# Optimization experiments

Hardware: AMD Instinct MI355X
Metric: run time of the kernel (lower is better)

Reference implementation:

```python
import jax, jax.numpy as jnp
import numpy as np

B, S, H, NH = 2, 2048, 1024, 16
HD = H // NH


def setup_inputs() -> dict:
    key = jax.random.key(0)
    ks = jax.random.split(key, 12)
    inp = {
        "query": jax.random.normal(ks[0], (B, S, H), dtype=jnp.float32),
        "key": jax.random.normal(ks[1], (B, S, H), dtype=jnp.float32),
        "value": jax.random.normal(ks[2], (B, S, H), dtype=jnp.float32),
        "mask": jnp.ones((B, 1, S, S), dtype=jnp.int32),
        "script_mask": jax.random.uniform(ks[3], (B, S, S), dtype=jnp.float32),
    }
    scale = 1.0 / np.sqrt(H)
    inp["Wq"] = jax.random.normal(ks[4], (H, H), dtype=jnp.float32) * scale
    inp["bq"] = jnp.zeros((H,), dtype=jnp.float32)
    inp["Wk"] = jax.random.normal(ks[5], (H, H), dtype=jnp.float32) * scale
    inp["bk"] = jnp.zeros((H,), dtype=jnp.float32)
    inp["Wv"] = jax.random.normal(ks[6], (H, H), dtype=jnp.float32) * scale
    inp["bv"] = jnp.zeros((H,), dtype=jnp.float32)
    inp["Wo"] = jax.random.normal(ks[7], (H, H), dtype=jnp.float32) * scale
    inp["bo"] = jnp.zeros((H,), dtype=jnp.float32)
    return inp


def reference(query, key, value, mask, script_mask, Wq, bq, Wk, bk, Wv, bv, Wo, bo):
    b, s, h = query.shape
    # projections; torch Linear: x @ W.T + b
    q = (query @ Wq.T + bq).reshape(b, s, NH, HD).transpose(0, 2, 1, 3)  # [b,nh,s,hd]
    k = (key @ Wk.T + bk).reshape(b, s, NH, HD).transpose(0, 2, 1, 3)
    v = (value @ Wv.T + bv).reshape(b, s, NH, HD).transpose(0, 2, 1, 3)
    scores = jnp.einsum("bhqd,bhkd->bhqk", q, k) / jnp.sqrt(jnp.float32(HD))
    # multiplicative script mask, broadcast over heads
    scores = scores * script_mask[:, None, :, :]
    # additive mask: positions where mask == 0 -> -inf
    scores = jnp.where(mask == 0, -jnp.inf, scores)
    attn = jax.nn.softmax(scores, axis=-1)
    out = jnp.einsum("bhqk,bhkd->bhqd", attn, v)  # [b,nh,s,hd]
    out = out.transpose(0, 2, 1, 3).reshape(b, s, h)
    return out @ Wo.T + bo
```

## Files before the change

kernel.cpp:

```cpp
#include <hip/hip_runtime.h>
#include <stdint.h>

#define NH 16
#define SEQ 2048
#define HDIM 1024

typedef short bf16x8 __attribute__((ext_vector_type(8)));
typedef float f32x4 __attribute__((ext_vector_type(4)));
typedef float f32x2 __attribute__((ext_vector_type(2)));

#define NEG_BIG (-1.0e30f)

static __device__ __forceinline__ uint32_t cvtpk_bf16(float lo, float hi) {
  uint32_t r;
  asm("v_cvt_pk_bf16_f32 %0, %1, %2" : "=v"(r) : "v"(lo), "v"(hi));
  return r;
}
static __device__ __forceinline__ uint16_t f2bf(float f) {
  return (uint16_t)cvtpk_bf16(f, f);
}
static __device__ __forceinline__ f32x2 pk_mul(f32x2 a, f32x2 b) {
  f32x2 d;
  asm("v_pk_mul_f32 %0, %1, %2" : "=v"(d) : "v"(a), "v"(b));
  return d;
}
static __device__ __forceinline__ f32x2 pk_add(f32x2 a, f32x2 b) {
  f32x2 d;
  asm("v_pk_add_f32 %0, %1, %2" : "=v"(d) : "v"(a), "v"(b));
  return d;
}
static __device__ __forceinline__ float bitf(uint32_t u) {
  return __builtin_bit_cast(float, u);
}

struct CvtArgs {
  const float* src[7];
  uint16_t* dst[7];
  int nblk[7];
};
__global__ __launch_bounds__(256) void cvt_bf16(CvtArgs a) {
  int ten = blockIdx.y;
  if (blockIdx.x >= a.nblk[ten]) return;
  size_t idx = ((size_t)blockIdx.x * 256 + threadIdx.x) * 8;
  const float* s = a.src[ten] + idx;
  float4 f0 = *(const float4*)(s);
  float4 f1 = *(const float4*)(s + 4);
  uint4 o;
  o.x = cvtpk_bf16(f0.x, f0.y);
  o.y = cvtpk_bf16(f0.z, f0.w);
  o.z = cvtpk_bf16(f1.x, f1.y);
  o.w = cvtpk_bf16(f1.z, f1.w);
  *(uint4*)(a.dst[ten] + idx) = o;
}

__global__ __launch_bounds__(256) void cm_prep(const int4* __restrict__ mask,
                                               const float4* __restrict__ sm,
                                               uint4* __restrict__ cm) {
  int i = blockIdx.x * 256 + threadIdx.x;
  int4 m0 = mask[2 * i];
  int4 m1 = mask[2 * i + 1];
  float4 s0 = sm[2 * i];
  float4 s1 = sm[2 * i + 1];
  const float cst = 0.18033688011112042f;
  auto pk = [&](int mA, int mB, float fa, float fb) -> uint32_t {
    float a = mA ? fa * cst : -1.0f;
    float b = mB ? fb * cst : -1.0f;
    return cvtpk_bf16(a, b);
  };
  uint4 o;
  o.x = pk(m0.x, m0.y, s0.x, s0.y);
  o.y = pk(m0.z, m0.w, s0.z, s0.w);
  o.z = pk(m1.x, m1.y, s1.x, s1.y);
  o.w = pk(m1.z, m1.w, s1.z, s1.w);
  cm[i] = o;
}

struct GemmArgs {
  const uint16_t* A[4];
  const uint16_t* B[4];
  const float* bias[4];
  void* C[4];
};

#define LDA 40

__global__ __launch_bounds__(256) void gemm_bt(GemmArgs ga, int modeBase) {
  int mode = modeBase + blockIdx.y;
  const uint16_t* __restrict__ A = ga.A[mode];
  const uint16_t* __restrict__ Bm = ga.B[mode];
  const float* __restrict__ bias = ga.bias[mode];

  int bid = blockIdx.x;
  int tm, tn;
  if (mode == 2) { tm = bid & 7; tn = bid >> 3; }
  else           { tm = bid >> 3; tn = bid & 7; }

  __shared__ uint16_t As[128 * LDA];
  __shared__ uint16_t Bs[128 * LDA];

  int t = threadIdx.x;
  int lane = t & 63, w = t >> 6;
  int quad = lane >> 4, lm = lane & 15;
  int wm = w >> 1, wn = w & 1;

  const uint16_t* Ab = A + (size_t)tm * 128 * 1024;
  const uint16_t* Bb = Bm + (size_t)tn * 128 * 1024;
  int srow = w * 32 + (lane >> 2);
  int scol = (lane & 3) * 8;

  f32x4 acc[4][4] = {};

  for (int kk = 0; kk < 1024; kk += 32) {
    uint4 a0 = *(const uint4*)(Ab + (size_t)srow * 1024 + kk + scol);
    uint4 a1 = *(const uint4*)(Ab + (size_t)(srow + 16) * 1024 + kk + scol);
    uint4 b0 = *(const uint4*)(Bb + (size_t)srow * 1024 + kk + scol);
    uint4 b1 = *(const uint4*)(Bb + (size_t)(srow + 16) * 1024 + kk + scol);
    __syncthreads();
    *(uint4*)&As[srow * LDA + scol] = a0;
    *(uint4*)&As[(srow + 16) * LDA + scol] = a1;
    *(uint4*)&Bs[srow * LDA + scol] = b0;
    *(uint4*)&Bs[(srow + 16) * LDA + scol] = b1;
    __syncthreads();

    bf16x8 af[4], bfr[4];
#pragma unroll
    for (int i = 0; i < 4; i++)
      af[i] = *(const bf16x8*)&As[(wm * 64 + i * 16 + lm) * LDA + quad * 8];
#pragma unroll
    for (int j = 0; j < 4; j++)
      bfr[j] = *(const bf16x8*)&Bs[(wn * 64 + j * 16 + lm) * LDA + quad * 8];
#pragma unroll
    for (int i = 0; i < 4; i++)
#pragma unroll
      for (int j = 0; j < 4; j++)
        acc[i][j] = __builtin_amdgcn_mfma_f32_16x16x32_bf16(af[i], bfr[j], acc[i][j], 0, 0, 0);
  }

  int rowb = tm * 128 + wm * 64;
  int colb = tn * 128 + wn * 64;
#pragma unroll
  for (int i = 0; i < 4; i++) {
#pragma unroll
    for (int j = 0; j < 4; j++) {
      int col = colb + j * 16 + lm;
#pragma unroll
      for (int r = 0; r < 4; r++) {
        int row = rowb + i * 16 + quad * 4 + r;
        float v = acc[i][j][r];
        if (mode == 2) {
          v += bias[row];
          int hh = row >> 6, hd = row & 63, b = col >> 11, s2 = col & 2047;
          ((uint16_t*)ga.C[2])[((size_t)((b * NH + hh) * 64 + hd) << 11) + s2] = f2bf(v);
        } else if (mode == 3) {
          v += bias[col];
          ((float*)ga.C[3])[(size_t)row * 1024 + col] = v;
        } else {
          v += bias[col];
          int b = row >> 11, s2 = row & 2047, hh = col >> 6, hd = col & 63;
          ((uint16_t*)ga.C[mode])[(((size_t)(b * NH + hh) * 2048 + s2) << 6) + hd] = f2bf(v);
        }
      }
    }
  }
}

#define LDK 72

__global__ __launch_bounds__(256) void attn(const uint16_t* __restrict__ qp,
                                            const uint16_t* __restrict__ kp,
                                            const uint16_t* __restrict__ vt,
                                            const uint16_t* __restrict__ cm,
                                            uint16_t* __restrict__ ao) {
  int h = blockIdx.x, qt = blockIdx.y, b = blockIdx.z;
  int t = threadIdx.x;
  int lane = t & 63, w = t >> 6;
  int quad = lane >> 4, c = lane & 15;

  __shared__ uint16_t Ks[64 * LDK];
  __shared__ uint16_t VTs[64 * LDK];
  __shared__ uint16_t Ps[64 * LDK];

  size_t bh = (size_t)(b * NH + h);
  const uint16_t* Kb = kp + bh * (SEQ * 64);
  const uint16_t* Vb = vt + bh * (64 * SEQ);
  const uint16_t* CMb = cm + ((size_t)b * SEQ + qt * 64) * SEQ;

  int qrow = qt * 64 + w * 16 + c;
  const uint16_t* Qb = qp + bh * (SEQ * 64) + (size_t)qrow * 64;
  bf16x8 qf0 = *(const bf16x8*)(Qb + quad * 8);
  bf16x8 qf1 = *(const bf16x8*)(Qb + 32 + quad * 8);

  f32x4 Oacc[4] = {};
  float m_run = NEG_BIG;
  float l_run = 0.0f;

  int krow = w * 8 + (lane >> 3);
  int kc = (lane & 7) * 8;

  const uint16_t* pK0 = Kb + (size_t)krow * 64 + kc;
  const uint16_t* pK1 = pK0 + 32 * 64;
  const uint16_t* pV0 = Vb + (size_t)krow * SEQ + kc;
  const uint16_t* pV1 = pV0 + (size_t)32 * SEQ;
  const uint16_t* pCM = CMb + (size_t)(w * 16 + c) * SEQ + quad * 4;

  uint16_t* sK0 = &Ks[krow * LDK + kc];
  uint16_t* sK1 = sK0 + 32 * LDK;
  uint16_t* sV0 = &VTs[krow * LDK + kc];
  uint16_t* sV1 = sV0 + 32 * LDK;

  const uint16_t* rK = &Ks[c * LDK];
  const uint16_t* rV = &VTs[c * LDK];
  uint16_t* sP = &Ps[(w * 16 + c) * LDK];
  int qo = quad * 8;

  auto compute = [&](uint2 c0, uint2 c1, uint2 c2, uint2 c3) {
    f32x4 st[4];
    __builtin_amdgcn_s_setprio(1);
#pragma unroll
    for (int i = 0; i < 4; i++) {
      bf16x8 a0 = *(const bf16x8*)(rK + i * 16 * LDK + qo);
      bf16x8 a1 = *(const bf16x8*)(rK + i * 16 * LDK + 32 + qo);
      f32x4 z = {};
      z = __builtin_amdgcn_mfma_f32_16x16x32_bf16(a0, qf0, z, 0, 0, 0);
      st[i] = __builtin_amdgcn_mfma_f32_16x16x32_bf16(a1, qf1, z, 0, 0, 0);
    }
    __builtin_amdgcn_s_setprio(0);

    const f32x2 big2 = {1.0e30f, 1.0e30f};
    f32x2 pp[8];
    float tmax = NEG_BIG;
    const uint2 cmv[4] = {c0, c1, c2, c3};
#pragma unroll
    for (int i = 0; i < 4; i++) {
      uint32_t w0 = cmv[i].x, w1 = cmv[i].y;
      f32x2 cf01 = {bitf(w0 << 16), bitf(w0 & 0xffff0000u)};
      f32x2 cf23 = {bitf(w1 << 16), bitf(w1 & 0xffff0000u)};
      f32x2 s01 = {st[i][0], st[i][1]};
      f32x2 s23 = {st[i][2], st[i][3]};
      f32x2 m01 = pk_mul(s01, cf01), q01 = pk_mul(big2, cf01);
      f32x2 m23 = pk_mul(s23, cf23), q23 = pk_mul(big2, cf23);
      f32x2 r01 = {fminf(m01.x, q01.x), fminf(m01.y, q01.y)};
      f32x2 r23 = {fminf(m23.x, q23.x), fminf(m23.y, q23.y)};
      pp[2 * i] = r01;
      pp[2 * i + 1] = r23;
      tmax = fmaxf(tmax, fmaxf(fmaxf(r01.x, r01.y), fmaxf(r23.x, r23.y)));
    }
    tmax = fmaxf(tmax, __shfl_xor(tmax, 16));
    tmax = fmaxf(tmax, __shfl_xor(tmax, 32));
    if (!__all(tmax <= m_run + 8.0f)) {
      float m_new = fmaxf(m_run, tmax);
      float alpha = exp2f(m_run - m_new);
      m_run = m_new;
      l_run *= alpha;
#pragma unroll
      for (int i = 0; i < 4; i++) Oacc[i] *= alpha;
    }
    f32x2 mneg = {-m_run, -m_run};
    f32x2 acc2 = {0.0f, 0.0f};
#pragma unroll
    for (int j = 0; j < 8; j++) {
      f32x2 e = pk_add(pp[j], mneg);
      pp[j].x = exp2f(e.x);
      pp[j].y = exp2f(e.y);
      acc2 = pk_add(acc2, pp[j]);
    }
    l_run += acc2.x + acc2.y;

#pragma unroll
    for (int i = 0; i < 4; i++) {
      uint2 pkd;
      pkd.x = cvtpk_bf16(pp[2 * i].x, pp[2 * i].y);
      pkd.y = cvtpk_bf16(pp[2 * i + 1].x, pp[2 * i + 1].y);
      *(uint2*)(sP + i * 16 + quad * 4) = pkd;
    }
    asm volatile("s_waitcnt lgkmcnt(0)" ::: "memory");
    __builtin_amdgcn_sched_barrier(0);

    bf16x8 pf0 = *(const bf16x8*)(sP + qo);
    bf16x8 pf1 = *(const bf16x8*)(sP + 32 + qo);
    __builtin_amdgcn_s_setprio(1);
#pragma unroll
    for (int i = 0; i < 4; i++) {
      bf16x8 v0 = *(const bf16x8*)(rV + i * 16 * LDK + qo);
      bf16x8 v1 = *(const bf16x8*)(rV + i * 16 * LDK + 32 + qo);
      Oacc[i] = __builtin_amdgcn_mfma_f32_16x16x32_bf16(v0, pf0, Oacc[i], 0, 0, 0);
      Oacc[i] = __builtin_amdgcn_mfma_f32_16x16x32_bf16(v1, pf1, Oacc[i], 0, 0, 0);
    }
    __builtin_amdgcn_s_setprio(0);
  };

  uint4 rk0 = *(const uint4*)(pK0), rk1 = *(const uint4*)(pK1);
  uint4 rv0 = *(const uint4*)(pV0), rv1 = *(const uint4*)(pV1);
  uint2 cA0 = *(const uint2*)(pCM);
  uint2 cA1 = *(const uint2*)(pCM + 16);
  uint2 cA2 = *(const uint2*)(pCM + 32);
  uint2 cA3 = *(const uint2*)(pCM + 48);
  pK0 += 64 * 64; pK1 += 64 * 64; pV0 += 64; pV1 += 64; pCM += 64;
  uint2 cB0, cB1, cB2, cB3;

  for (int it = 0; it < SEQ / 128; ++it) {
    __syncthreads();
    *(uint4*)sK0 = rk0;
    *(uint4*)sK1 = rk1;
    *(uint4*)sV0 = rv0;
    *(uint4*)sV1 = rv1;
    __syncthreads();
    rk0 = *(const uint4*)(pK0); rk1 = *(const uint4*)(pK1);
    rv0 = *(const uint4*)(pV0); rv1 = *(const uint4*)(pV1);
    cB0 = *(const uint2*)(pCM);
    cB1 = *(const uint2*)(pCM + 16);
    cB2 = *(const uint2*)(pCM + 32);
    cB3 = *(const uint2*)(pCM + 48);
    pK0 += 64 * 64; pK1 += 64 * 64; pV0 += 64; pV1 += 64; pCM += 64;
    compute(cA0, cA1, cA2, cA3);
    __syncthreads();
    *(uint4*)sK0 = rk0;
    *(uint4*)sK1 = rk1;
    *(uint4*)sV0 = rv0;
    *(uint4*)sV1 = rv1;
    __syncthreads();
    if (it < SEQ / 128 - 1) {
      rk0 = *(const uint4*)(pK0); rk1 = *(const uint4*)(pK1);
      rv0 = *(const uint4*)(pV0); rv1 = *(const uint4*)(pV1);
      cA0 = *(const uint2*)(pCM);
      cA1 = *(const uint2*)(pCM + 16);
      cA2 = *(const uint2*)(pCM + 32);
      cA3 = *(const uint2*)(pCM + 48);
      pK0 += 64 * 64; pK1 += 64 * 64; pV0 += 64; pV1 += 64; pCM += 64;
    }
    compute(cB0, cB1, cB2, cB3);
  }

  float lf = l_run + __shfl_xor(l_run, 16);
  lf = lf + __shfl_xor(lf, 32);
  float inv = 1.0f / lf;
  uint16_t* Ob = ao + ((size_t)(b * SEQ) + qt * 64 + w * 16 + c) * HDIM + h * 64;
#pragma unroll
  for (int i = 0; i < 4; i++) {
    uint2 ov;
    ov.x = cvtpk_bf16(Oacc[i][0] * inv, Oacc[i][1] * inv);
    ov.y = cvtpk_bf16(Oacc[i][2] * inv, Oacc[i][3] * inv);
    *(uint2*)(Ob + i * 16 + quad * 4) = ov;
  }
}

extern "C" void kernel_launch(void* const* d_in, const int* in_sizes, int n_in,
                              void* d_out, int out_size, void* d_ws, size_t ws_size,
                              hipStream_t stream) {
  (void)in_sizes; (void)n_in; (void)out_size; (void)ws_size;
  const float* query = (const float*)d_in[0];
  const float* key   = (const float*)d_in[1];
  const float* value = (const float*)d_in[2];
  const int*   mask  = (const int*)d_in[3];
  const float* smask = (const float*)d_in[4];
  const float* Wq = (const float*)d_in[5];
  const float* bq = (const float*)d_in[6];
  const float* Wk = (const float*)d_in[7];
  const float* bk = (const float*)d_in[8];
  const float* Wv = (const float*)d_in[9];
  const float* bv = (const float*)d_in[10];
  const float* Wo = (const float*)d_in[11];
  const float* bo = (const float*)d_in[12];

  char* p = (char*)d_ws;
  uint16_t* xq  = (uint16_t*)p; p += (size_t)2 * SEQ * HDIM * 2;
  uint16_t* xk  = (uint16_t*)p; p += (size_t)2 * SEQ * HDIM * 2;
  uint16_t* xv  = (uint16_t*)p; p += (size_t)2 * SEQ * HDIM * 2;
  uint16_t* wqb = (uint16_t*)p; p += (size_t)HDIM * HDIM * 2;
  uint16_t* wkb = (uint16_t*)p; p += (size_t)HDIM * HDIM * 2;
  uint16_t* wvb = (uint16_t*)p; p += (size_t)HDIM * HDIM * 2;
  uint16_t* wob = (uint16_t*)p; p += (size_t)HDIM * HDIM * 2;
  uint16_t* qp  = (uint16_t*)p; p += (size_t)2 * NH * SEQ * 64 * 2;
  uint16_t* kpp = (uint16_t*)p; p += (size_t)2 * NH * SEQ * 64 * 2;
  uint16_t* vtp = (uint16_t*)p; p += (size_t)2 * NH * SEQ * 64 * 2;
  uint16_t* cmw = (uint16_t*)p; p += (size_t)2 * SEQ * SEQ * 2;
  uint16_t* aob = (uint16_t*)p; p += (size_t)2 * SEQ * HDIM * 2;

  CvtArgs ca;
  ca.src[0] = query; ca.dst[0] = xq;  ca.nblk[0] = 2048;
  ca.src[1] = key;   ca.dst[1] = xk;  ca.nblk[1] = 2048;
  ca.src[2] = value; ca.dst[2] = xv;  ca.nblk[2] = 2048;
  ca.src[3] = Wq;    ca.dst[3] = wqb; ca.nblk[3] = 512;
  ca.src[4] = Wk;    ca.dst[4] = wkb; ca.nblk[4] = 512;
  ca.src[5] = Wv;    ca.dst[5] = wvb; ca.nblk[5] = 512;
  ca.src[6] = Wo;    ca.dst[6] = wob; ca.nblk[6] = 512;
  cvt_bf16<<<dim3(2048, 7), 256, 0, stream>>>(ca);

  cm_prep<<<4096, 256, 0, stream>>>((const int4*)mask, (const float4*)smask, (uint4*)cmw);

  GemmArgs ga;
  ga.A[0] = xq;  ga.B[0] = wqb; ga.bias[0] = bq; ga.C[0] = qp;
  ga.A[1] = xk;  ga.B[1] = wkb; ga.bias[1] = bk; ga.C[1] = kpp;
  ga.A[2] = wvb; ga.B[2] = xv;  ga.bias[2] = bv; ga.C[2] = vtp;
  ga.A[3] = aob; ga.B[3] = wob; ga.bias[3] = bo; ga.C[3] = d_out;

  gemm_bt<<<dim3(256, 3), 256, 0, stream>>>(ga, 0);
  attn<<<dim3(NH, SEQ / 64, 2), 256, 0, stream>>>(qp, kpp, vtp, cmw, aob);
  gemm_bt<<<dim3(256, 1), 256, 0, stream>>>(ga, 3);
}
```

Baseline: 390.4 us.

## Use direct global-to-LDS loads in GEMM and drop attention register prefetch

The projection GEMM now stages its A and B tiles with global_load_lds, which writes straight into LDS without passing through VGPRs. The padded row stride is removed, so the shared tiles become unpadded 32-element rows. Separately, the attention kernel's two-stage register prefetch of K, V and the mask is replaced by a simple loop that loads and then stores each tile before computing. This cuts register pressure and code size, but gives up the overlap between global loads and compute, and the unpadded GEMM layout may raise LDS bank conflicts.

```diff
diff --git a/kernel.cpp b/kernel.cpp
--- a/kernel.cpp
+++ b/kernel.cpp
@@ -31,6 +31,11 @@
 }
 static __device__ __forceinline__ float bitf(uint32_t u) {
   return __builtin_bit_cast(float, u);
+}
+static __device__ __forceinline__ void gload_lds16(const void* g, void* l) {
+  __builtin_amdgcn_global_load_lds(
+      (const __attribute__((address_space(1))) void*)g,
+      (__attribute__((address_space(3))) void*)l, 16, 0, 0);
 }
 
 struct CvtArgs {
@@ -82,8 +87,6 @@
   void* C[4];
 };
 
-#define LDA 40
-
 __global__ __launch_bounds__(256) void gemm_bt(GemmArgs ga, int modeBase) {
   int mode = modeBase + blockIdx.y;
   const uint16_t* __restrict__ A = ga.A[mode];
@@ -95,8 +98,8 @@
   if (mode == 2) { tm = bid & 7; tn = bid >> 3; }
   else           { tm = bid >> 3; tn = bid & 7; }
 
-  __shared__ uint16_t As[128 * LDA];
-  __shared__ uint16_t Bs[128 * LDA];
+  __shared__ uint16_t As[128 * 32];
+  __shared__ uint16_t Bs[128 * 32];
 
   int t = threadIdx.x;
   int lane = t & 63, w = t >> 6;
@@ -105,30 +108,36 @@
 
   const uint16_t* Ab = A + (size_t)tm * 128 * 1024;
   const uint16_t* Bb = Bm + (size_t)tn * 128 * 1024;
-  int srow = w * 32 + (lane >> 2);
+
+  int srow = lane >> 2;
   int scol = (lane & 3) * 8;
+  const uint16_t* gA0 = Ab + (size_t)(w * 32 + srow) * 1024 + scol;
+  const uint16_t* gA1 = gA0 + 16 * 1024;
+  const uint16_t* gB0 = Bb + (size_t)(w * 32 + srow) * 1024 + scol;
+  const uint16_t* gB1 = gB0 + 16 * 1024;
+  uint16_t* lA0 = &As[(w * 32) * 32];
+  uint16_t* lA1 = &As[(w * 32 + 16) * 32];
+  uint16_t* lB0 = &Bs[(w * 32) * 32];
+  uint16_t* lB1 = &Bs[(w * 32 + 16) * 32];
 
   f32x4 acc[4][4] = {};
 
   for (int kk = 0; kk < 1024; kk += 32) {
-    uint4 a0 = *(const uint4*)(Ab + (size_t)srow * 1024 + kk + scol);
-    uint4 a1 = *(const uint4*)(Ab + (size_t)(srow + 16) * 1024 + kk + scol);
-    uint4 b0 = *(const uint4*)(Bb + (size_t)srow * 1024 + kk + scol);
-    uint4 b1 = *(const uint4*)(Bb + (size_t)(srow + 16) * 1024 + kk + scol);
     __syncthreads();
-    *(uint4*)&As[srow * LDA + scol] = a0;
-    *(uint4*)&As[(srow + 16) * LDA + scol] = a1;
-    *(uint4*)&Bs[srow * LDA + scol] = b0;
-    *(uint4*)&Bs[(srow + 16) * LDA + scol] = b1;
+    gload_lds16(gA0, lA0);
+    gload_lds16(gA1, lA1);
+    gload_lds16(gB0, lB0);
+    gload_lds16(gB1, lB1);
+    gA0 += 32; gA1 += 32; gB0 += 32; gB1 += 32;
     __syncthreads();
 
     bf16x8 af[4], bfr[4];
 #pragma unroll
     for (int i = 0; i < 4; i++)
-      af[i] = *(const bf16x8*)&As[(wm * 64 + i * 16 + lm) * LDA + quad * 8];
+      af[i] = *(const bf16x8*)&As[(wm * 64 + i * 16 + lm) * 32 + quad * 8];
 #pragma unroll
     for (int j = 0; j < 4; j++)
-      bfr[j] = *(const bf16x8*)&Bs[(wn * 64 + j * 16 + lm) * LDA + quad * 8];
+      bfr[j] = *(const bf16x8*)&Bs[(wn * 64 + j * 16 + lm) * 32 + quad * 8];
 #pragma unroll
     for (int i = 0; i < 4; i++)
 #pragma unroll
@@ -213,7 +222,23 @@
   uint16_t* sP = &Ps[(w * 16 + c) * LDK];
   int qo = quad * 8;
 
-  auto compute = [&](uint2 c0, uint2 c1, uint2 c2, uint2 c3) {
+  for (int kt = 0; kt < SEQ; kt += 64) {
+    uint2 cm0 = *(const uint2*)(pCM);
+    uint2 cm1 = *(const uint2*)(pCM + 16);
+    uint2 cm2 = *(const uint2*)(pCM + 32);
+    uint2 cm3 = *(const uint2*)(pCM + 48);
+    uint4 k0  = *(const uint4*)(pK0);
+    uint4 k1  = *(const uint4*)(pK1);
+    uint4 v0g = *(const uint4*)(pV0);
+    uint4 v1g = *(const uint4*)(pV1);
+    pCM += 64; pK0 += 64 * 64; pK1 += 64 * 64; pV0 += 64; pV1 += 64;
+    __syncthreads();
+    *(uint4*)sK0 = k0;
+    *(uint4*)sK1 = k1;
+    *(uint4*)sV0 = v0g;
+    *(uint4*)sV1 = v1g;
+    __syncthreads();
+
     f32x4 st[4];
     __builtin_amdgcn_s_setprio(1);
 #pragma unroll
@@ -229,7 +254,7 @@
     const f32x2 big2 = {1.0e30f, 1.0e30f};
     f32x2 pp[8];
     float tmax = NEG_BIG;
-    const uint2 cmv[4] = {c0, c1, c2, c3};
+    const uint2 cmv[4] = {cm0, cm1, cm2, cm3};
 #pragma unroll
     for (int i = 0; i < 4; i++) {
       uint32_t w0 = cmv[i].x, w1 = cmv[i].y;
@@ -287,48 +312,6 @@
       Oacc[i] = __builtin_amdgcn_mfma_f32_16x16x32_bf16(v1, pf1, Oacc[i], 0, 0, 0);
     }
     __builtin_amdgcn_s_setprio(0);
-  };
-
-  uint4 rk0 = *(const uint4*)(pK0), rk1 = *(const uint4*)(pK1);
-  uint4 rv0 = *(const uint4*)(pV0), rv1 = *(const uint4*)(pV1);
-  uint2 cA0 = *(const uint2*)(pCM);
-  uint2 cA1 = *(const uint2*)(pCM + 16);
-  uint2 cA2 = *(const uint2*)(pCM + 32);
-  uint2 cA3 = *(const uint2*)(pCM + 48);
-  pK0 += 64 * 64; pK1 += 64 * 64; pV0 += 64; pV1 += 64; pCM += 64;
-  uint2 cB0, cB1, cB2, cB3;
-
-  for (int it = 0; it < SEQ / 128; ++it) {
-    __syncthreads();
-    *(uint4*)sK0 = rk0;
-    *(uint4*)sK1 = rk1;
-    *(uint4*)sV0 = rv0;
-    *(uint4*)sV1 = rv1;
-    __syncthreads();
-    rk0 = *(const uint4*)(pK0); rk1 = *(const uint4*)(pK1);
-    rv0 = *(const uint4*)(pV0); rv1 = *(const uint4*)(pV1);
-    cB0 = *(const uint2*)(pCM);
-    cB1 = *(const uint2*)(pCM + 16);
-    cB2 = *(const uint2*)(pCM + 32);
-    cB3 = *(const uint2*)(pCM + 48);
-    pK0 += 64 * 64; pK1 += 64 * 64; pV0 += 64; pV1 += 64; pCM += 64;
-    compute(cA0, cA1, cA2, cA3);
-    __syncthreads();
-    *(uint4*)sK0 = rk0;
-    *(uint4*)sK1 = rk1;
-    *(uint4*)sV0 = rv0;
-    *(uint4*)sV1 = rv1;
-    __syncthreads();
-    if (it < SEQ / 128 - 1) {
-      rk0 = *(const uint4*)(pK0); rk1 = *(const uint4*)(pK1);
-      rv0 = *(const uint4*)(pV0); rv1 = *(const uint4*)(pV1);
-      cA0 = *(const uint2*)(pCM);
-      cA1 = *(const uint2*)(pCM + 16);
-      cA2 = *(const uint2*)(pCM + 32);
-      cA3 = *(const uint2*)(pCM + 48);
-      pK0 += 64 * 64; pK1 += 64 * 64; pV0 += 64; pV1 += 64; pCM += 64;
-    }
-    compute(cB0, cB1, cB2, cB3);
   }
 
   float lf = l_run + __shfl_xor(l_run, 16);
```

Result: faster. 352.3 us (-9.7%).
